# Performance work log

Hardware: AMD Instinct MI355X
Metric: run time of the kernel (lower is better)

Reference implementation:

```python
import jax, jax.numpy as jnp
import numpy as np

DIM = 512
NSLOTS = 8
ITERS = 3
EPS = 1e-8
LN_EPS = 1e-5
SCALE = DIM ** -0.5


def _ln(x, g, b):
    m = jnp.mean(x, axis=-1, keepdims=True)
    v = jnp.mean((x - m) ** 2, axis=-1, keepdims=True)
    return (x - m) / jnp.sqrt(v + LN_EPS) * g + b


def _gru(x, h, W_ih, W_hh, b_ih, b_hh):
    # PyTorch GRUCell, gate order r,z,n
    gi = x @ W_ih.T + b_ih
    gh = h @ W_hh.T + b_hh
    ir, iz, inn = jnp.split(gi, 3, axis=-1)
    hr, hz, hn = jnp.split(gh, 3, axis=-1)
    r = jax.nn.sigmoid(ir + hr)
    z = jax.nn.sigmoid(iz + hz)
    n = jnp.tanh(inn + r * hn)
    return (1.0 - z) * n + z * h


def _norm_attn(dots):
    # softmax over slot axis, then renormalize over token axis
    a = jax.nn.softmax(dots, axis=1)
    return a / (jnp.sum(a, axis=-1, keepdims=True) + EPS)


def setup_inputs() -> dict:
    key = jax.random.key(0)
    ks = jax.random.split(key, 16)
    b, na, ni = 32, 1024, 3136
    d, hd = DIM, DIM  # hidden_dim = max(dim, 128) = 512
    s = 0.02
    inp = {
        'inputs_audio': jax.random.normal(ks[0], (b, na, d), jnp.float32),
        'inputs_image': jax.random.normal(ks[1], (b, ni, d), jnp.float32),
        'slots_noise': jax.random.normal(ks[2], (b, NSLOTS, d), jnp.float32),
        'slots_mu': jax.random.normal(ks[3], (1, 1, d), jnp.float32),
        'slots_logsigma': jnp.zeros((1, 1, d), jnp.float32),
        'ln_in_g': jnp.ones((d,), jnp.float32), 'ln_in_b': jnp.zeros((d,), jnp.float32),
        'ln_slots_g': jnp.ones((d,), jnp.float32), 'ln_slots_b': jnp.zeros((d,), jnp.float32),
        'ln_ff_g': jnp.ones((d,), jnp.float32), 'ln_ff_b': jnp.zeros((d,), jnp.float32),
        'Wq': jax.random.normal(ks[4], (d, d), jnp.float32) * s, 'bq': jnp.zeros((d,), jnp.float32),
        'Wk': jax.random.normal(ks[5], (d, d), jnp.float32) * s, 'bk': jnp.zeros((d,), jnp.float32),
        'Wv': jax.random.normal(ks[6], (d, d), jnp.float32) * s, 'bv': jnp.zeros((d,), jnp.float32),
        'W_ih': jax.random.normal(ks[7], (3 * d, d), jnp.float32) * s,
        'W_hh': jax.random.normal(ks[8], (3 * d, d), jnp.float32) * s,
        'b_ih': jnp.zeros((3 * d,), jnp.float32), 'b_hh': jnp.zeros((3 * d,), jnp.float32),
        'W1': jax.random.normal(ks[9], (hd, d), jnp.float32) * s, 'b1': jnp.zeros((hd,), jnp.float32),
        'W2': jax.random.normal(ks[10], (d, hd), jnp.float32) * s, 'b2': jnp.zeros((d,), jnp.float32),
    }
    return inp


def reference(inputs_audio, inputs_image, slots_noise, slots_mu, slots_logsigma,
              ln_in_g, ln_in_b, ln_slots_g, ln_slots_b, ln_ff_g, ln_ff_b,
              Wq, bq, Wk, bk, Wv, bv, W_ih, W_hh, b_ih, b_hh, W1, b1, W2, b2):
    b, na, d = inputs_audio.shape
    slots0 = slots_mu + jnp.exp(slots_logsigma) * slots_noise  # [b, S, d]

    ia = _ln(inputs_audio, ln_in_g, ln_in_b)
    ii = _ln(inputs_image, ln_in_g, ln_in_b)
    k_a = ia @ Wk.T + bk
    v_a = ia @ Wv.T + bv
    k_i = ii @ Wk.T + bk
    v_i = ii @ Wv.T + bv

    def mlp(x):
        return jax.nn.relu(x @ W1.T + b1) @ W2.T + b2

    def step(slots, k, v):
        prev = slots
        sn = _ln(slots, ln_slots_g, ln_slots_b)
        q = sn @ Wq.T + bq
        dots = jnp.einsum('bid,bjd->bij', q, k) * SCALE
        attn = _norm_attn(dots)
        upd = jnp.einsum('bjd,bij->bid', v, attn)
        h = _gru(upd.reshape(-1, d), prev.reshape(-1, d), W_ih, W_hh, b_ih, b_hh)
        slots = h.reshape(b, -1, d)
        slots = slots + mlp(_ln(slots, ln_ff_g, ln_ff_b))
        return slots, q, attn

    slots_a, slots_i = slots0, slots0
    for _ in range(ITERS):
        slots_a, q_a, attn_a = step(slots_a, k_a, v_a)
        slots_i, q_i, attn_i = step(slots_i, k_i, v_i)

    cross_ai = _norm_attn(jnp.einsum('bid,bjd->bij', q_a, k_i) * SCALE)  # audio->image
    cross_ia = _norm_attn(jnp.einsum('bid,bjd->bij', q_i, k_a) * SCALE)  # image->audio

    return (slots_a, q_a, k_a, attn_a, cross_ia,
            slots_i, q_i, k_i, attn_i, cross_ai)
```

## Files before the change

### kernel.cpp

```cpp
#include <hip/hip_runtime.h>
#include <hip/hip_bf16.h>

#define DIM 512
#define EPS 1e-8f
#define LN_EPS 1e-5f
#define SCALE 0.04419417382415922f

typedef float f32x4 __attribute__((ext_vector_type(4)));
typedef __bf16 bf16;
typedef __bf16 bf16x8 __attribute__((ext_vector_type(8)));

typedef const __attribute__((address_space(1))) void gvoid;
typedef __attribute__((address_space(3))) void lvoid;

__device__ inline float bf2f_lo(unsigned u) { union { unsigned x; float f; } c; c.x = u << 16; return c.f; }
__device__ inline float bf2f_hi(unsigned u) { union { unsigned x; float f; } c; c.x = u & 0xffff0000u; return c.f; }

#define SBAR() do { __builtin_amdgcn_sched_barrier(0); \
                    __builtin_amdgcn_s_barrier(); \
                    __builtin_amdgcn_sched_barrier(0); } while (0)

__global__ __launch_bounds__(256) void k_stats_convert(
    const float* __restrict__ xa, const float* __restrict__ xi,
    bf16* __restrict__ xbfa, bf16* __restrict__ xbfi,
    float* __restrict__ sa, float* __restrict__ si, int MA)
{
  int row = blockIdx.x * 4 + (threadIdx.x >> 6);
  int lane = threadIdx.x & 63;
  bool isA = row < MA;
  int lrow = isA ? row : row - MA;
  const float* xr = (isA ? xa : xi) + (size_t)lrow * DIM;
  bf16* xbf = (isA ? xbfa : xbfi) + (size_t)lrow * DIM;
  float* stats = (isA ? sa : si) + (size_t)lrow * 2;
  float4 a = *(const float4*)(xr + lane * 8);
  float4 b = *(const float4*)(xr + lane * 8 + 4);
  float s  = a.x + a.y + a.z + a.w + b.x + b.y + b.z + b.w;
  float ss = a.x*a.x + a.y*a.y + a.z*a.z + a.w*a.w
           + b.x*b.x + b.y*b.y + b.z*b.z + b.w*b.w;
  for (int off = 32; off; off >>= 1) { s += __shfl_xor(s, off); ss += __shfl_xor(ss, off); }
  float mean = s * (1.0f / DIM);
  float var  = ss * (1.0f / DIM) - mean * mean;
  float rs   = rsqrtf(var + LN_EPS);
  if (lane == 0) { stats[0] = mean; stats[1] = rs; }
  union { bf16 h[8]; uint4 u; } cv;
  cv.h[0] = (bf16)a.x; cv.h[1] = (bf16)a.y; cv.h[2] = (bf16)a.z; cv.h[3] = (bf16)a.w;
  cv.h[4] = (bf16)b.x; cv.h[5] = (bf16)b.y; cv.h[6] = (bf16)b.z; cv.h[7] = (bf16)b.w;
  *(uint4*)(xbf + lane * 8) = cv.u;
}

__global__ __launch_bounds__(256) void k_stats512(
    const float* __restrict__ x, float* __restrict__ stats)
{
  int row = blockIdx.x * 4 + (threadIdx.x >> 6);
  int lane = threadIdx.x & 63;
  const float* xr = x + (size_t)row * DIM;
  float4 a = *(const float4*)(xr + lane * 8);
  float4 b = *(const float4*)(xr + lane * 8 + 4);
  float s  = a.x + a.y + a.z + a.w + b.x + b.y + b.z + b.w;
  float ss = a.x*a.x + a.y*a.y + a.z*a.z + a.w*a.w
           + b.x*b.x + b.y*b.y + b.z*b.z + b.w*b.w;
  for (int off = 32; off; off >>= 1) { s += __shfl_xor(s, off); ss += __shfl_xor(ss, off); }
  float mean = s * (1.0f / DIM);
  float rs   = rsqrtf(ss * (1.0f / DIM) - mean * mean + LN_EPS);
  if (lane == 0) { stats[row * 2] = mean; stats[row * 2 + 1] = rs; }
}

__global__ __launch_bounds__(64) void k_prep(
    const float* __restrict__ Wk, const float* __restrict__ bk,
    const float* __restrict__ Wv, const float* __restrict__ bv,
    const float* __restrict__ g_in, const float* __restrict__ b_in,
    const float* __restrict__ Wq, const float* __restrict__ bq,
    const float* __restrict__ g_s, const float* __restrict__ b_s,
    const float* __restrict__ W1, const float* __restrict__ b1,
    const float* __restrict__ g_f, const float* __restrict__ b_f,
    bf16* __restrict__ wbf, float* __restrict__ c1kv, float* __restrict__ c2kv,
    float* __restrict__ Wqp, float* __restrict__ cq1, float* __restrict__ cq2,
    float* __restrict__ W1p, float* __restrict__ cf1, float* __restrict__ cf2)
{
  int n = blockIdx.x; int lane = threadIdx.x;
  if (n < 1024) {
    const float* W = (n < DIM) ? (Wk + (size_t)n * DIM) : (Wv + (size_t)(n - DIM) * DIM);
    float bias = (n < DIM) ? bk[n] : bv[n - DIM];
    float s1 = 0.f, s2 = 0.f;
    union { bf16 h[8]; uint4 u; } cv;
#pragma unroll
    for (int j = 0; j < 8; ++j) {
      int d = lane * 8 + j;
      float w = W[d];
      float gw = g_in[d] * w;
      s1 += gw; s2 += b_in[d] * w;
      cv.h[j] = (bf16)gw;
    }
    *(uint4*)(wbf + (size_t)n * DIM + lane * 8) = cv.u;
    for (int off = 32; off; off >>= 1) { s1 += __shfl_xor(s1, off); s2 += __shfl_xor(s2, off); }
    if (lane == 0) { c1kv[n] = s1; c2kv[n] = s2 + bias; }
  } else {
    int m; const float* W; float bias; const float* g; const float* b;
    float* Wp; float* cc1; float* cc2;
    if (n < 1536) { m = n - 1024; W = Wq + (size_t)m * DIM; bias = bq[m]; g = g_s; b = b_s; Wp = Wqp; cc1 = cq1; cc2 = cq2; }
    else          { m = n - 1536; W = W1 + (size_t)m * DIM; bias = b1[m]; g = g_f; b = b_f; Wp = W1p; cc1 = cf1; cc2 = cf2; }
    float s1 = 0.f, s2 = 0.f;
    float arr[8];
#pragma unroll
    for (int j = 0; j < 8; ++j) {
      int d = lane * 8 + j;
      float w = W[d];
      float gw = g[d] * w;
      s1 += gw; s2 += b[d] * w;
      arr[j] = gw;
    }
    *(float4*)(Wp + (size_t)m * DIM + lane * 8)     = make_float4(arr[0], arr[1], arr[2], arr[3]);
    *(float4*)(Wp + (size_t)m * DIM + lane * 8 + 4) = make_float4(arr[4], arr[5], arr[6], arr[7]);
    for (int off = 32; off; off >>= 1) { s1 += __shfl_xor(s1, off); s2 += __shfl_xor(s2, off); }
    if (lane == 0) { cc1[m] = s1; cc2[m] = s2 + bias; }
  }
}

__global__ __launch_bounds__(256, 3) void k_kv_gemm(
    const bf16* __restrict__ xa, const bf16* __restrict__ xi,
    const bf16* __restrict__ wbf,
    const float* __restrict__ sa, const float* __restrict__ si,
    const float* __restrict__ c1, const float* __restrict__ c2,
    float* __restrict__ ka, float* __restrict__ ki,
    bf16* __restrict__ kba, bf16* __restrict__ kbi,
    bf16* __restrict__ va, bf16* __restrict__ vi,
    int nblkA, int nblkTot)
{
  __shared__ bf16 As[3][128 * 32];
  __shared__ bf16 Bs[3][128 * 32];
  const int t = threadIdx.x, wave = t >> 6, lane = t & 63;
  int bid = blockIdx.x;
  int rid = (bid & 7) * (nblkTot >> 3) + (bid >> 3);
  bool isA = rid < nblkA;
  int lrid = isA ? rid : rid - nblkA;
  const bf16* x = isA ? xa : xi;
  const float* stats = isA ? sa : si;
  float* kout = isA ? ka : ki;
  bf16* kbf = isA ? kba : kbi;
  bf16* vbf = isA ? va : vi;
  const int row0 = (lrid >> 3) * 128, col0 = (lrid & 7) * 128;
  f32x4 acc[4][4] = {};

  const int sr  = wave * 16 + (lane >> 2);
  const int sgl = ((lane & 3) ^ ((lane >> 3) & 3)) * 8;
  const bf16* asrc = x   + (size_t)(row0 + sr) * DIM + sgl;
  const bf16* bsrc = wbf + (size_t)(col0 + sr) * DIM + sgl;

  auto stage = [&](int buf, int k0) {
#pragma unroll
    for (int p = 0; p < 2; ++p) {
      __builtin_amdgcn_global_load_lds(
          (gvoid*)(asrc + (size_t)(p * 64) * DIM + k0),
          (lvoid*)((char*)&As[0][0] + buf * 8192 + (p * 256 + wave * 64) * 16), 16, 0, 0);
      __builtin_amdgcn_global_load_lds(
          (gvoid*)(bsrc + (size_t)(p * 64) * DIM + k0),
          (lvoid*)((char*)&Bs[0][0] + buf * 8192 + (p * 256 + wave * 64) * 16), 16, 0, 0);
    }
  };

  const int l15 = lane & 15, q16 = lane >> 4;
  const int wm = wave >> 1, wn = wave & 1;
  const int gpx = (q16 ^ ((l15 >> 1) & 3)) * 8;

  stage(0, 0);
  stage(1, 32);
  stage(2, 64);
  asm volatile("s_waitcnt vmcnt(8)" ::: "memory");
  SBAR();
  int cur = 0;
  for (int ks = 0; ks < 16; ++ks) {
    const bf16* Ab = &As[0][0] + cur * (128 * 32);
    const bf16* Bb = &Bs[0][0] + cur * (128 * 32);
    bf16x8 ax[4], bw[4];
#pragma unroll
    for (int mi = 0; mi < 4; ++mi)
      ax[mi] = *(const bf16x8*)(Ab + (wm * 64 + mi * 16 + l15) * 32 + gpx);
#pragma unroll
    for (int ni = 0; ni < 4; ++ni)
      bw[ni] = *(const bf16x8*)(Bb + (wn * 64 + ni * 16 + l15) * 32 + gpx);
    __builtin_amdgcn_s_setprio(1);
#pragma unroll
    for (int ni = 0; ni < 4; ++ni)
#pragma unroll
      for (int mi = 0; mi < 4; ++mi)
        acc[ni][mi] = __builtin_amdgcn_mfma_f32_16x16x32_bf16(bw[ni], ax[mi], acc[ni][mi], 0, 0, 0);
    __builtin_amdgcn_s_setprio(0);
    if (ks == 15) break;
    SBAR();
    if (ks < 13) {
      stage(cur, (ks + 3) * 32);
      asm volatile("s_waitcnt vmcnt(8)" ::: "memory");
    } else if (ks == 13) {
      asm volatile("s_waitcnt vmcnt(4)" ::: "memory");
    } else {
      asm volatile("s_waitcnt vmcnt(0)" ::: "memory");
    }
    SBAR();
    cur = (cur == 2) ? 0 : cur + 1;
  }

#pragma unroll
  for (int mi = 0; mi < 4; ++mi) {
    int row = row0 + wm * 64 + mi * 16 + l15;
    float2 st = *(const float2*)&stats[row * 2];
    float rs = st.y, rm = st.y * st.x;
#pragma unroll
    for (int ni = 0; ni < 4; ++ni) {
      int col = col0 + wn * 64 + ni * 16 + q16 * 4;
      float4 c1v = *(const float4*)&c1[col];
      float4 c2v = *(const float4*)&c2[col];
      f32x4 a = acc[ni][mi];
      float4 o;
      o.x = rs * a[0] - rm * c1v.x + c2v.x;
      o.y = rs * a[1] - rm * c1v.y + c2v.y;
      o.z = rs * a[2] - rm * c1v.z + c2v.z;
      o.w = rs * a[3] - rm * c1v.w + c2v.w;
      union { bf16 h[4]; uint2 u; } pk;
      pk.h[0] = (bf16)o.x; pk.h[1] = (bf16)o.y; pk.h[2] = (bf16)o.z; pk.h[3] = (bf16)o.w;
      if (col0 < DIM) {
        *(float4*)&kout[(size_t)row * DIM + col] = o;
        if (kbf) *(uint2*)&kbf[(size_t)row * DIM + col] = pk.u;
      } else {
        *(uint2*)&vbf[(size_t)row * DIM + (col - DIM)] = pk.u;
      }
    }
  }
}

__global__ __launch_bounds__(256) void k_f2bf(
    const float* __restrict__ in, bf16* __restrict__ out)
{
  size_t i = ((size_t)blockIdx.x * 256 + threadIdx.x) * 8;
  float4 a = *(const float4*)(in + i);
  float4 b = *(const float4*)(in + i + 4);
  union { bf16 h[8]; uint4 u; } cv;
  cv.h[0] = (bf16)a.x; cv.h[1] = (bf16)a.y; cv.h[2] = (bf16)a.z; cv.h[3] = (bf16)a.w;
  cv.h[4] = (bf16)b.x; cv.h[5] = (bf16)b.y; cv.h[6] = (bf16)b.z; cv.h[7] = (bf16)b.w;
  *(uint4*)(out + i) = cv.u;
}

__global__ __launch_bounds__(256) void k_init_slots(
    const float* __restrict__ noise, const float* __restrict__ mu,
    const float* __restrict__ lsig, float* __restrict__ slots,
    float* __restrict__ stats)
{
  int row = blockIdx.x;
  int t = threadIdx.x;
  int d1 = t + 256;
  float v0 = mu[t]  + expf(lsig[t])  * noise[row * DIM + t];
  float v1 = mu[d1] + expf(lsig[d1]) * noise[row * DIM + d1];
  slots[(size_t)row * DIM + t]  = v0;
  slots[(size_t)row * DIM + d1] = v1;
  slots[131072 + (size_t)row * DIM + t]  = v0;
  slots[131072 + (size_t)row * DIM + d1] = v1;
  float s = v0 + v1, ss = v0 * v0 + v1 * v1;
  for (int off = 32; off; off >>= 1) { s += __shfl_xor(s, off); ss += __shfl_xor(ss, off); }
  __shared__ float red[8];
  int wv = t >> 6, ln = t & 63;
  if (ln == 0) { red[wv] = s; red[4 + wv] = ss; }
  __syncthreads();
  if (t == 0) {
    s = red[0] + red[1] + red[2] + red[3];
    ss = red[4] + red[5] + red[6] + red[7];
    float mean = s * (1.0f / DIM);
    float rs = rsqrtf(ss * (1.0f / DIM) - mean * mean + LN_EPS);
    stats[row * 2] = mean; stats[row * 2 + 1] = rs;
    stats[(row + 256) * 2] = mean; stats[(row + 256) * 2 + 1] = rs;
  }
}

template <int MODE>
__global__ __launch_bounds__(128) void k_sgemm(
    const float* __restrict__ A, const float* __restrict__ B, int N,
    float* __restrict__ C,
    const float* __restrict__ c1a, const float* __restrict__ c2a,
    const float* __restrict__ stats,
    const float* __restrict__ bias, const float* __restrict__ invden,
    const float* __restrict__ R,
    float* __restrict__ outA, float* __restrict__ outI,
    bf16* __restrict__ qbf)
{
  __shared__ float As[32][33];
  __shared__ float Bs[64][33];
  int t = threadIdx.x;
  int m0 = blockIdx.y * 32, n0 = blockIdx.x * 64;
  float acc[4][4] = {};
  for (int k0 = 0; k0 < DIM; k0 += 32) {
    __syncthreads();
#pragma unroll
    for (int p = 0; p < 2; ++p) {
      int idx = p * 128 + t, r = idx >> 3, c4 = (idx & 7) * 4;
      float4 v = *(const float4*)(A + (size_t)(m0 + r) * DIM + k0 + c4);
      As[r][c4] = v.x; As[r][c4 + 1] = v.y; As[r][c4 + 2] = v.z; As[r][c4 + 3] = v.w;
    }
#pragma unroll
    for (int p = 0; p < 4; ++p) {
      int idx = p * 128 + t, r = idx >> 3, c4 = (idx & 7) * 4;
      float4 v = *(const float4*)(B + (size_t)(n0 + r) * DIM + k0 + c4);
      Bs[r][c4] = v.x; Bs[r][c4 + 1] = v.y; Bs[r][c4 + 2] = v.z; Bs[r][c4 + 3] = v.w;
    }
    __syncthreads();
    int tr = t >> 4, tc = t & 15;
#pragma unroll
    for (int k = 0; k < 32; ++k) {
      float a0 = As[tr * 4][k], a1 = As[tr * 4 + 1][k], a2 = As[tr * 4 + 2][k], a3 = As[tr * 4 + 3][k];
      float b0 = Bs[tc * 4][k], b1 = Bs[tc * 4 + 1][k], b2 = Bs[tc * 4 + 2][k], b3 = Bs[tc * 4 + 3][k];
      acc[0][0] += a0 * b0; acc[0][1] += a0 * b1; acc[0][2] += a0 * b2; acc[0][3] += a0 * b3;
      acc[1][0] += a1 * b0; acc[1][1] += a1 * b1; acc[1][2] += a1 * b2; acc[1][3] += a1 * b3;
      acc[2][0] += a2 * b0; acc[2][1] += a2 * b1; acc[2][2] += a2 * b2; acc[2][3] += a2 * b3;
      acc[3][0] += a3 * b0; acc[3][1] += a3 * b1; acc[3][2] += a3 * b2; acc[3][3] += a3 * b3;
    }
  }
  int tr = t >> 4, tc = t & 15;
#pragma unroll
  for (int mi = 0; mi < 4; ++mi) {
    int row = m0 + tr * 4 + mi;
#pragma unroll
    for (int ni = 0; ni < 4; ++ni) {
      int col = n0 + tc * 4 + ni;
      float v = acc[mi][ni];
      if (MODE == 0 || MODE == 3) {
        float mean = stats[row * 2], rs = stats[row * 2 + 1];
        v = rs * v - rs * mean * c1a[col] + c2a[col];
      }
      if (MODE == 4) v += bias[col];
      if (MODE == 3) v = fmaxf(v, 0.0f);
      if (MODE == 4) v += R[(size_t)row * N + col];
      if (MODE == 0) {
        if (row < 256) outA[(size_t)row * DIM + col] = v;
        else           outI[(size_t)(row - 256) * DIM + col] = v;
        qbf[(size_t)row * DIM + col] = (bf16)(v * SCALE);
      } else {
        C[(size_t)row * N + col] = v;
        if (MODE == 4 && outA) {
          if (row < 256) outA[(size_t)row * DIM + col] = v;
          else           outI[(size_t)(row - 256) * DIM + col] = v;
        }
      }
    }
  }
}

__global__ __launch_bounds__(128) void k_gates(
    const float* __restrict__ num, const float* __restrict__ slots,
    const float* __restrict__ Wih, const float* __restrict__ Whh,
    const float* __restrict__ bih, const float* __restrict__ bhh,
    const float* __restrict__ invden,
    float* __restrict__ gib, float* __restrict__ ghb)
{
  bool first = blockIdx.x < 24;
  const float* A = first ? num : slots;
  const float* B = first ? Wih : Whh;
  const float* bias = first ? bih : bhh;
  float* C = first ? gib : ghb;
  int n0 = (first ? blockIdx.x : blockIdx.x - 24) * 64;
  int m0 = blockIdx.y * 32;
  __shared__ float As[32][33];
  __shared__ float Bs[64][33];
  int t = threadIdx.x;
  float acc[4][4] = {};
  for (int k0 = 0; k0 < DIM; k0 += 32) {
    __syncthreads();
#pragma unroll
    for (int p = 0; p < 2; ++p) {
      int idx = p * 128 + t, r = idx >> 3, c4 = (idx & 7) * 4;
      float4 v = *(const float4*)(A + (size_t)(m0 + r) * DIM + k0 + c4);
      As[r][c4] = v.x; As[r][c4 + 1] = v.y; As[r][c4 + 2] = v.z; As[r][c4 + 3] = v.w;
    }
#pragma unroll
    for (int p = 0; p < 4; ++p) {
      int idx = p * 128 + t, r = idx >> 3, c4 = (idx & 7) * 4;
      float4 v = *(const float4*)(B + (size_t)(n0 + r) * DIM + k0 + c4);
      Bs[r][c4] = v.x; Bs[r][c4 + 1] = v.y; Bs[r][c4 + 2] = v.z; Bs[r][c4 + 3] = v.w;
    }
    __syncthreads();
    int tr = t >> 4, tc = t & 15;
#pragma unroll
    for (int k = 0; k < 32; ++k) {
      float a0 = As[tr * 4][k], a1 = As[tr * 4 + 1][k], a2 = As[tr * 4 + 2][k], a3 = As[tr * 4 + 3][k];
      float b0 = Bs[tc * 4][k], b1 = Bs[tc * 4 + 1][k], b2 = Bs[tc * 4 + 2][k], b3 = Bs[tc * 4 + 3][k];
      acc[0][0] += a0 * b0; acc[0][1] += a0 * b1; acc[0][2] += a0 * b2; acc[0][3] += a0 * b3;
      acc[1][0] += a1 * b0; acc[1][1] += a1 * b1; acc[1][2] += a1 * b2; acc[1][3] += a1 * b3;
      acc[2][0] += a2 * b0; acc[2][1] += a2 * b1; acc[2][2] += a2 * b2; acc[2][3] += a2 * b3;
      acc[3][0] += a3 * b0; acc[3][1] += a3 * b1; acc[3][2] += a3 * b2; acc[3][3] += a3 * b3;
    }
  }
  int tr = t >> 4, tc = t & 15;
#pragma unroll
  for (int mi = 0; mi < 4; ++mi) {
    int row = m0 + tr * 4 + mi;
    float sc = first ? invden[row] : 1.0f;
#pragma unroll
    for (int ni = 0; ni < 4; ++ni) {
      int col = n0 + tc * 4 + ni;
      C[(size_t)row * 1536 + col] = acc[mi][ni] * sc + bias[col];
    }
  }
}

__global__ __launch_bounds__(256, 3) void k_dots(
    const bf16* __restrict__ qA, const bf16* __restrict__ qI,
    const bf16* __restrict__ kA, const bf16* __restrict__ kI,
    float* __restrict__ aoutA, float* __restrict__ aoutI,
    float* __restrict__ denp, int NA_, int NI_)
{
  __shared__ bf16 ks[3][128 * 64];
  __shared__ float dsh[32];
  int t = threadIdx.x, wave = t >> 6, lane = t & 63;
  int b = blockIdx.y, tile = blockIdx.x;
  bool isA = tile < 8;
  int til = isA ? tile : tile - 8;
  int N = isA ? NA_ : NI_;
  int j0 = til * 128;
  const bf16* q = (isA ? qA : qI) + (size_t)b * 8 * DIM;
  const bf16* k = (isA ? kA : kI) + (size_t)b * N * DIM;
  float* aout = (isA ? aoutA : aoutI) + (size_t)b * 8 * N;
  int drow = (isA ? 0 : 256) + b * 8;

  const int l15 = lane & 15, q16 = lane >> 4;
  bf16x8 afq[16];
  {
    const bf16* qr = q + (size_t)(l15 & 7) * DIM + q16 * 8;
#pragma unroll
    for (int f = 0; f < 16; ++f)
      afq[f] = *(const bf16x8*)(qr + f * 32);
  }

  const int sr  = wave * 8 + (lane >> 3);
  const int sgl = ((lane & 7) ^ (lane >> 3)) * 8;
  int jr = j0 + sr; if (jr > N - 1) jr = N - 1;
  const bf16* ksrc = k + (size_t)jr * DIM + sgl;
  int jr2 = j0 + 32 + sr; if (jr2 > N - 1) jr2 = N - 1;
  const bf16* ksrc2 = k + (size_t)jr2 * DIM + sgl;
  int jr3 = j0 + 64 + sr; if (jr3 > N - 1) jr3 = N - 1;
  const bf16* ksrc3 = k + (size_t)jr3 * DIM + sgl;
  int jr4 = j0 + 96 + sr; if (jr4 > N - 1) jr4 = N - 1;
  const bf16* ksrc4 = k + (size_t)jr4 * DIM + sgl;

  auto stage = [&](int buf, int c) {
    __builtin_amdgcn_global_load_lds((gvoid*)(ksrc  + c * 64),
        (lvoid*)((char*)&ks[0][0] + buf * 16384 + (0 * 256 + wave * 64) * 16), 16, 0, 0);
    __builtin_amdgcn_global_load_lds((gvoid*)(ksrc2 + c * 64),
        (lvoid*)((char*)&ks[0][0] + buf * 16384 + (1 * 256 + wave * 64) * 16), 16, 0, 0);
    __builtin_amdgcn_global_load_lds((gvoid*)(ksrc3 + c * 64),
        (lvoid*)((char*)&ks[0][0] + buf * 16384 + (2 * 256 + wave * 64) * 16), 16, 0, 0);
    __builtin_amdgcn_global_load_lds((gvoid*)(ksrc4 + c * 64),
        (lvoid*)((char*)&ks[0][0] + buf * 16384 + (3 * 256 + wave * 64) * 16), 16, 0, 0);
  };

  stage(0, 0);
  stage(1, 1);
  stage(2, 2);
  asm volatile("s_waitcnt vmcnt(8)" ::: "memory");
  SBAR();
  f32x4 acc[2] = {};
  int cur = 0;
  for (int c = 0; c < 8; ++c) {
    const bf16* kb = &ks[0][0] + cur * (128 * 64);
    __builtin_amdgcn_s_setprio(1);
#pragma unroll
    for (int kk = 0; kk < 2; ++kk) {
#pragma unroll
      for (int n = 0; n < 2; ++n) {
        int R = wave * 32 + n * 16 + l15;
        int gp = (kk * 4 + q16) ^ (R & 7);
        bf16x8 bfr = *(const bf16x8*)(kb + R * 64 + gp * 8);
        acc[n] = __builtin_amdgcn_mfma_f32_16x16x32_bf16(afq[c * 2 + kk], bfr, acc[n], 0, 0, 0);
      }
    }
    __builtin_amdgcn_s_setprio(0);
    if (c == 7) break;
    SBAR();
    if (c < 5) {
      stage(cur, c + 3);
      asm volatile("s_waitcnt vmcnt(8)" ::: "memory");
    } else if (c == 5) {
      asm volatile("s_waitcnt vmcnt(4)" ::: "memory");
    } else {
      asm volatile("s_waitcnt vmcnt(0)" ::: "memory");
    }
    SBAR();
    cur = (cur == 2) ? 0 : cur + 1;
  }

  float dsum[8];
#pragma unroll
  for (int i = 0; i < 8; ++i) dsum[i] = 0.f;
#pragma unroll
  for (int n = 0; n < 2; ++n) {
    int j = j0 + wave * 32 + n * 16 + l15;
    float dv[8];
#pragma unroll
    for (int r = 0; r < 4; ++r) {
      float own = acc[n][r];
      float oth = __shfl_xor(own, 16);
      if (q16 == 0) { dv[r] = own; dv[4 + r] = oth; }
      else          { dv[r] = oth; dv[4 + r] = own; }
    }
    float mx = dv[0];
#pragma unroll
    for (int i = 1; i < 8; ++i) mx = fmaxf(mx, dv[i]);
    float sum = 0.f;
#pragma unroll
    for (int i = 0; i < 8; ++i) { dv[i] = __expf(dv[i] - mx); sum += dv[i]; }
    float inv = 1.0f / sum;
    bool valid = (j < N);
#pragma unroll
    for (int i = 0; i < 8; ++i) {
      float av = valid ? dv[i] * inv : 0.0f;
      dsum[i] += av;
      if (valid && q16 == 0) aout[(size_t)i * N + j] = av;
    }
  }
#pragma unroll
  for (int i = 0; i < 8; ++i) {
    float v = dsum[i];
    v += __shfl_xor(v, 1); v += __shfl_xor(v, 2);
    v += __shfl_xor(v, 4); v += __shfl_xor(v, 8);
    dsum[i] = v;
  }
  if (lane == 0) {
#pragma unroll
    for (int i = 0; i < 8; ++i) dsh[wave * 8 + i] = dsum[i];
  }
  __syncthreads();
  if (t < 8) {
    float den = dsh[t] + dsh[8 + t] + dsh[16 + t] + dsh[24 + t];
    denp[((size_t)drow + t) * 32 + til] = den;
  }
}

__global__ __launch_bounds__(256) void k_upd(
    const bf16* __restrict__ vA, const bf16* __restrict__ vI,
    const float* __restrict__ aA, const float* __restrict__ aI,
    float* __restrict__ numpA, float* __restrict__ numpI, int NA_, int NI_)
{
  __shared__ float ash[128 * 12];
  int t = threadIdx.x, b = blockIdx.y, x = blockIdx.x;
  bool isA = x < 4;
  int c = isA ? x : x - 4;
  int N = isA ? NA_ : NI_;
  int nc = isA ? 4 : 13;
  int jstart = c * 256;
  int jend = jstart + 256; if (jend > N) jend = N;
  const bf16* v = (isA ? vA : vI) + (size_t)b * N * DIM;
  const float* a = (isA ? aA : aI) + (size_t)b * 8 * N;
  float acc[16] = {};
  int d0 = t * 2;
  for (int jt = jstart; jt < jend; jt += 128) {
    int jmax = jend - jt; if (jmax > 128) jmax = 128;
    __syncthreads();
    {
      int i = t >> 5, jq = (t & 31) * 4;
      float4 av = make_float4(0.f, 0.f, 0.f, 0.f);
      if (jt + jq < N) av = *(const float4*)&a[(size_t)i * N + jt + jq];
      ash[(jq + 0) * 12 + i] = av.x;
      ash[(jq + 1) * 12 + i] = av.y;
      ash[(jq + 2) * 12 + i] = av.z;
      ash[(jq + 3) * 12 + i] = av.w;
    }
    __syncthreads();
    for (int jj = 0; jj < jmax; ++jj) {
      unsigned vv = *(const unsigned*)(v + (size_t)(jt + jj) * DIM + d0);
      float v0 = bf2f_lo(vv), v1 = bf2f_hi(vv);
      float4 a0 = *(const float4*)&ash[jj * 12];
      float4 a1 = *(const float4*)&ash[jj * 12 + 4];
      acc[0]  += a0.x * v0; acc[1]  += a0.x * v1;
      acc[2]  += a0.y * v0; acc[3]  += a0.y * v1;
      acc[4]  += a0.z * v0; acc[5]  += a0.z * v1;
      acc[6]  += a0.w * v0; acc[7]  += a0.w * v1;
      acc[8]  += a1.x * v0; acc[9]  += a1.x * v1;
      acc[10] += a1.y * v0; acc[11] += a1.y * v1;
      acc[12] += a1.z * v0; acc[13] += a1.z * v1;
      acc[14] += a1.w * v0; acc[15] += a1.w * v1;
    }
  }
  float* np = (isA ? numpA : numpI) + (((size_t)b * nc + c) * 8) * DIM;
#pragma unroll
  for (int i = 0; i < 8; ++i)
    *(float2*)&np[(size_t)i * DIM + d0] = make_float2(acc[i * 2], acc[i * 2 + 1]);
}

__global__ __launch_bounds__(256) void k_numred(
    const float* __restrict__ numpA, const float* __restrict__ numpI,
    const float* __restrict__ denp,
    float* __restrict__ num, float* __restrict__ invden)
{
  int m = blockIdx.x, t = threadIdx.x;
  bool isA = m < 256;
  int mm = isA ? m : m - 256;
  int bb = mm >> 3, i = mm & 7;
  int nc = isA ? 4 : 13;
  const float* np = (isA ? numpA : numpI) + (((size_t)bb * nc) * 8 + i) * DIM;
  int d0 = t * 2;
  float s0 = 0.f, s1 = 0.f;
  for (int c = 0; c < nc; ++c) {
    float2 vv = *(const float2*)&np[(size_t)c * 8 * DIM + d0];
    s0 += vv.x; s1 += vv.y;
  }
  *(float2*)&num[(size_t)m * DIM + d0] = make_float2(s0, s1);
  if (t == 0) {
    int nch = isA ? 8 : 25;
    float den = EPS;
    for (int c2 = 0; c2 < nch; ++c2) den += denp[(size_t)m * 32 + c2];
    invden[m] = 1.0f / den;
  }
}

__global__ __launch_bounds__(256) void k_gru(
    const float* __restrict__ gi, const float* __restrict__ gh,
    const float* __restrict__ prev,
    float* __restrict__ hout, float* __restrict__ stats_h)
{
  int m = blockIdx.x; int t = threadIdx.x;
  size_t b3 = (size_t)m * 1536, b1 = (size_t)m * DIM;
  float h[2]; float s = 0.f, ss = 0.f;
#pragma unroll
  for (int p = 0; p < 2; ++p) {
    int d = t + p * 256;
    float ir = gi[b3 + d], iz = gi[b3 + 512 + d], in_ = gi[b3 + 1024 + d];
    float hr = gh[b3 + d], hz = gh[b3 + 512 + d], hn = gh[b3 + 1024 + d];
    float r = 1.f / (1.f + __expf(-(ir + hr)));
    float z = 1.f / (1.f + __expf(-(iz + hz)));
    float n = tanhf(in_ + r * hn);
    float hv = (1.f - z) * n + z * prev[b1 + d];
    hout[b1 + d] = hv;
    h[p] = hv; s += hv; ss += hv * hv;
  }
  for (int off = 32; off; off >>= 1) { s += __shfl_xor(s, off); ss += __shfl_xor(ss, off); }
  __shared__ float red[8];
  int wv = t >> 6, ln = t & 63;
  if (ln == 0) { red[wv] = s; red[4 + wv] = ss; }
  __syncthreads();
  s = red[0] + red[1] + red[2] + red[3];
  ss = red[4] + red[5] + red[6] + red[7];
  float mean = s * (1.0f / DIM);
  float rs = rsqrtf(ss * (1.0f / DIM) - mean * mean + LN_EPS);
  if (t == 0) { stats_h[m * 2] = mean; stats_h[m * 2 + 1] = rs; }
}

__global__ __launch_bounds__(256) void k_renorm2(
    const float* __restrict__ aA, const float* __restrict__ aI,
    const float* __restrict__ denp,
    float* __restrict__ outA, float* __restrict__ outI, int NA_, int NI_)
{
  int m = blockIdx.x; int t = threadIdx.x;
  bool isA = m < 256;
  int mm = isA ? m : m - 256;
  int N = isA ? NA_ : NI_;
  int nch = isA ? 8 : 25;
  const float* in = (isA ? aA : aI) + (size_t)mm * N;
  float* out = (isA ? outA : outI) + (size_t)mm * N;
  float den = EPS;
  for (int c = 0; c < nch; ++c) den += denp[(size_t)m * 32 + c];
  float inv = 1.0f / den;
  for (int idx = t; idx * 4 < N; idx += 256) {
    float4 v = *(const float4*)&in[idx * 4];
    v.x *= inv; v.y *= inv; v.z *= inv; v.w *= inv;
    *(float4*)&out[idx * 4] = v;
  }
}

extern "C" void kernel_launch(void* const* d_in, const int* in_sizes, int n_in,
                              void* d_out, int out_size, void* d_ws, size_t ws_size,
                              hipStream_t stream)
{
  (void)in_sizes; (void)n_in; (void)out_size;
  const float* x_a   = (const float*)d_in[0];
  const float* x_i   = (const float*)d_in[1];
  const float* noise = (const float*)d_in[2];
  const float* mu    = (const float*)d_in[3];
  const float* lsig  = (const float*)d_in[4];
  const float* ln_in_g = (const float*)d_in[5];
  const float* ln_in_b = (const float*)d_in[6];
  const float* ln_s_g  = (const float*)d_in[7];
  const float* ln_s_b  = (const float*)d_in[8];
  const float* ln_f_g  = (const float*)d_in[9];
  const float* ln_f_b  = (const float*)d_in[10];
  const float* Wq = (const float*)d_in[11]; const float* bq = (const float*)d_in[12];
  const float* Wk = (const float*)d_in[13]; const float* bk = (const float*)d_in[14];
  const float* Wv = (const float*)d_in[15]; const float* bv = (const float*)d_in[16];
  const float* W_ih = (const float*)d_in[17]; const float* W_hh = (const float*)d_in[18];
  const float* b_ih = (const float*)d_in[19]; const float* b_hh = (const float*)d_in[20];
  const float* W1 = (const float*)d_in[21]; const float* b1 = (const float*)d_in[22];
  const float* W2 = (const float*)d_in[23]; const float* b2 = (const float*)d_in[24];

  const int NA = 1024, NI = 3136;
  const int MA = 32 * NA, MI = 32 * NI;

  float* out = (float*)d_out;
  float* o_slots_a  = out;
  float* o_q_a      = out + 131072;
  float* o_k_a      = out + 262144;
  float* o_attn_a   = out + 17039360;
  float* o_cross_ia = out + 17301504;
  float* o_slots_i  = out + 17563648;
  float* o_q_i      = out + 17694720;
  float* o_k_i      = out + 17825792;
  float* o_attn_i   = out + 69206016;
  float* o_cross_ai = out + 70008832;

  char* w = (char*)d_ws;
  size_t used = 0;
  auto alloc = [&](size_t bytes) {
    char* p = w + used;
    used += (bytes + 255) & ~(size_t)255;
    return p;
  };
  bf16* xbf_a = (bf16*)alloc((size_t)MA * DIM * 2);
  bf16* xbf_i = (bf16*)alloc((size_t)MI * DIM * 2);
  bf16* vbf_a = (bf16*)alloc((size_t)MA * DIM * 2);
  bf16* vbf_i = (bf16*)alloc((size_t)MI * DIM * 2);
  float* stats_a = (float*)alloc((size_t)MA * 2 * 4);
  float* stats_i = (float*)alloc((size_t)MI * 2 * 4);
  bf16* wbf  = (bf16*)alloc(1024 * 512 * 2);
  float* c1kv = (float*)alloc(1024 * 4);
  float* c2kv = (float*)alloc(1024 * 4);
  float* Wqp = (float*)alloc(512 * 512 * 4);
  float* cq1 = (float*)alloc(512 * 4);
  float* cq2 = (float*)alloc(512 * 4);
  float* W1p = (float*)alloc(512 * 512 * 4);
  float* cf1 = (float*)alloc(512 * 4);
  float* cf2 = (float*)alloc(512 * 4);
  float* slots = (float*)alloc(512 * 512 * 4);
  bf16*  qbf   = (bf16*)alloc(512 * 512 * 2);
  float* mid   = (float*)alloc(512 * 512 * 4);
  float* hid   = (float*)alloc(512 * 512 * 4);
  float* num   = (float*)alloc(512 * 512 * 4);
  float* gib   = (float*)alloc(512 * 1536 * 4);
  float* ghb   = (float*)alloc(512 * 1536 * 4);
  float* stats_s = (float*)alloc(512 * 2 * 4);
  float* stats_h = (float*)alloc(512 * 2 * 4);
  float* invden  = (float*)alloc(512 * 4);
  float* denp    = (float*)alloc(512 * 32 * 4);
  float* abuf_a  = (float*)alloc((size_t)256 * NA * 4);
  float* abuf_i  = (float*)alloc((size_t)256 * NI * 4);
  float* numpA   = (float*)alloc((size_t)32 * 4 * 8 * DIM * 4);
  float* numpI   = (float*)alloc((size_t)32 * 13 * 8 * DIM * 4);
  if (used > ws_size) return;

  size_t kbf_bytes = (((size_t)MA * DIM * 2 + 255) & ~(size_t)255)
                   + (((size_t)MI * DIM * 2 + 255) & ~(size_t)255);
  bf16* kbf_a; bf16* kbf_i; bool kbf_fused;
  if (used + kbf_bytes <= ws_size) {
    kbf_a = (bf16*)alloc((size_t)MA * DIM * 2);
    kbf_i = (bf16*)alloc((size_t)MI * DIM * 2);
    kbf_fused = true;
  } else {
    kbf_a = xbf_a; kbf_i = xbf_i;
    kbf_fused = false;
  }

  k_stats_convert<<<(MA + MI) / 4, 256, 0, stream>>>(x_a, x_i, xbf_a, xbf_i,
                                                     stats_a, stats_i, MA);
  k_prep<<<2048, 64, 0, stream>>>(Wk, bk, Wv, bv, ln_in_g, ln_in_b,
                                  Wq, bq, ln_s_g, ln_s_b, W1, b1, ln_f_g, ln_f_b,
                                  wbf, c1kv, c2kv, Wqp, cq1, cq2, W1p, cf1, cf2);
  {
    int nblkA = (MA / 128) * 8;
    int nblkTot = nblkA + (MI / 128) * 8;
    k_kv_gemm<<<nblkTot, 256, 0, stream>>>(xbf_a, xbf_i, wbf, stats_a, stats_i,
        c1kv, c2kv, o_k_a, o_k_i,
        kbf_fused ? kbf_a : nullptr, kbf_fused ? kbf_i : nullptr,
        vbf_a, vbf_i, nblkA, nblkTot);
  }
  if (!kbf_fused) {
    k_f2bf<<<MA * DIM / 2048, 256, 0, stream>>>(o_k_a, kbf_a);
    k_f2bf<<<MI * DIM / 2048, 256, 0, stream>>>(o_k_i, kbf_i);
  }
  k_init_slots<<<256, 256, 0, stream>>>(noise, mu, lsig, slots, stats_s);

  for (int it = 0; it < 3; ++it) {
    bool last = (it == 2);
    k_sgemm<0><<<dim3(8, 16), 128, 0, stream>>>(slots, Wqp, DIM, nullptr,
        cq1, cq2, stats_s, nullptr, nullptr, nullptr, o_q_a, o_q_i, qbf);
    k_dots<<<dim3(33, 32), 256, 0, stream>>>(qbf, qbf + 256 * DIM,
        kbf_a, kbf_i, abuf_a, abuf_i, denp, NA, NI);
    k_upd<<<dim3(17, 32), 256, 0, stream>>>(vbf_a, vbf_i, abuf_a, abuf_i, numpA, numpI, NA, NI);
    k_numred<<<512, 256, 0, stream>>>(numpA, numpI, denp, num, invden);
    k_gates<<<dim3(48, 16), 128, 0, stream>>>(num, slots, W_ih, W_hh,
        b_ih, b_hh, invden, gib, ghb);
    k_gru<<<512, 256, 0, stream>>>(gib, ghb, slots, mid, stats_h);
    k_sgemm<3><<<dim3(8, 16), 128, 0, stream>>>(mid, W1p, DIM, hid,
        cf1, cf2, stats_h, nullptr, nullptr, nullptr, nullptr, nullptr, nullptr);
    k_sgemm<4><<<dim3(8, 16), 128, 0, stream>>>(hid, W2, DIM, slots,
        nullptr, nullptr, nullptr, b2, nullptr, mid,
        last ? o_slots_a : nullptr, last ? o_slots_i : nullptr, nullptr);
    if (!last) k_stats512<<<128, 256, 0, stream>>>(slots, stats_s);
  }

  k_renorm2<<<512, 256, 0, stream>>>(abuf_a, abuf_i, denp, o_attn_a, o_attn_i, NA, NI);

  k_dots<<<dim3(33, 32), 256, 0, stream>>>(qbf + 256 * DIM, qbf,
      kbf_a, kbf_i, abuf_a, abuf_i, denp, NA, NI);
  k_renorm2<<<512, 256, 0, stream>>>(abuf_a, abuf_i, denp, o_cross_ia, o_cross_ai, NA, NI);
}
```

Before: 1.121 ms.

## Fuse dots and update kernels, compute cross-attention in final iteration, double-buffer GEMMs

Merges the attention-dots kernel and the attention-times-V update kernel into one kernel that keeps the attention tile in shared memory. This removes the full attention write and read on the first two iterations. On the last iteration it also computes the cross-attention logits against the same staged K tile, so the separate cross dots pass no longer has to re-read K. The KV GEMM and dots pipelines drop from triple to double buffering to cut LDS use and raise occupancy. The trade-offs are a shallower prefetch pipeline and more partial numerator chunks for the reduction kernel to sum.

New measurement: 1.104 ms. About the same (-1.5%).

```diff
diff --git a/kernel.cpp b/kernel.cpp
--- a/kernel.cpp
+++ b/kernel.cpp
@@ -116,7 +116,7 @@
   }
 }
 
-__global__ __launch_bounds__(256, 3) void k_kv_gemm(
+__global__ __launch_bounds__(256, 4) void k_kv_gemm(
     const bf16* __restrict__ xa, const bf16* __restrict__ xi,
     const bf16* __restrict__ wbf,
     const float* __restrict__ sa, const float* __restrict__ si,
@@ -126,8 +126,8 @@
     bf16* __restrict__ va, bf16* __restrict__ vi,
     int nblkA, int nblkTot)
 {
-  __shared__ bf16 As[3][128 * 32];
-  __shared__ bf16 Bs[3][128 * 32];
+  __shared__ bf16 As[2][128 * 32];
+  __shared__ bf16 Bs[2][128 * 32];
   const int t = threadIdx.x, wave = t >> 6, lane = t & 63;
   int bid = blockIdx.x;
   int rid = (bid & 7) * (nblkTot >> 3) + (bid >> 3);
@@ -151,10 +151,10 @@
     for (int p = 0; p < 2; ++p) {
       __builtin_amdgcn_global_load_lds(
           (gvoid*)(asrc + (size_t)(p * 64) * DIM + k0),
-          (lvoid*)((char*)&As[0][0] + buf * 8192 + (p * 256 + wave * 64) * 16), 16, 0, 0);
+          (lvoid*)((char*)&As[buf][0] + (p * 256 + wave * 64) * 16), 16, 0, 0);
       __builtin_amdgcn_global_load_lds(
           (gvoid*)(bsrc + (size_t)(p * 64) * DIM + k0),
-          (lvoid*)((char*)&Bs[0][0] + buf * 8192 + (p * 256 + wave * 64) * 16), 16, 0, 0);
+          (lvoid*)((char*)&Bs[buf][0] + (p * 256 + wave * 64) * 16), 16, 0, 0);
     }
   };
 
@@ -164,13 +164,12 @@
 
   stage(0, 0);
   stage(1, 32);
-  stage(2, 64);
-  asm volatile("s_waitcnt vmcnt(8)" ::: "memory");
+  asm volatile("s_waitcnt vmcnt(4)" ::: "memory");
   SBAR();
   int cur = 0;
   for (int ks = 0; ks < 16; ++ks) {
-    const bf16* Ab = &As[0][0] + cur * (128 * 32);
-    const bf16* Bb = &Bs[0][0] + cur * (128 * 32);
+    const bf16* Ab = &As[cur][0];
+    const bf16* Bb = &Bs[cur][0];
     bf16x8 ax[4], bw[4];
 #pragma unroll
     for (int mi = 0; mi < 4; ++mi)
@@ -187,16 +186,14 @@
     __builtin_amdgcn_s_setprio(0);
     if (ks == 15) break;
     SBAR();
-    if (ks < 13) {
-      stage(cur, (ks + 3) * 32);
-      asm volatile("s_waitcnt vmcnt(8)" ::: "memory");
-    } else if (ks == 13) {
+    if (ks < 14) {
+      stage(cur, (ks + 2) * 32);
       asm volatile("s_waitcnt vmcnt(4)" ::: "memory");
     } else {
       asm volatile("s_waitcnt vmcnt(0)" ::: "memory");
     }
     SBAR();
-    cur = (cur == 2) ? 0 : cur + 1;
+    cur ^= 1;
   }
 
 #pragma unroll
@@ -327,8 +324,10 @@
       if (MODE == 3) v = fmaxf(v, 0.0f);
       if (MODE == 4) v += R[(size_t)row * N + col];
       if (MODE == 0) {
-        if (row < 256) outA[(size_t)row * DIM + col] = v;
-        else           outI[(size_t)(row - 256) * DIM + col] = v;
+        if (outA) {
+          if (row < 256) outA[(size_t)row * DIM + col] = v;
+          else           outI[(size_t)(row - 256) * DIM + col] = v;
+        }
         qbf[(size_t)row * DIM + col] = (bf16)(v * SCALE);
       } else {
         C[(size_t)row * N + col] = v;
@@ -398,32 +397,46 @@
   }
 }
 
-__global__ __launch_bounds__(256, 3) void k_dots(
+template <int LAST>
+__global__ __launch_bounds__(256) void k_dots_upd(
     const bf16* __restrict__ qA, const bf16* __restrict__ qI,
     const bf16* __restrict__ kA, const bf16* __restrict__ kI,
+    const bf16* __restrict__ vA, const bf16* __restrict__ vI,
     float* __restrict__ aoutA, float* __restrict__ aoutI,
-    float* __restrict__ denp, int NA_, int NI_)
-{
-  __shared__ bf16 ks[3][128 * 64];
-  __shared__ float dsh[32];
+    float* __restrict__ acA, float* __restrict__ acI,
+    float* __restrict__ denp, float* __restrict__ denpc,
+    float* __restrict__ numpA, float* __restrict__ numpI,
+    int NA_, int NI_)
+{
+  __shared__ bf16 ks[2][128 * 64];
+  __shared__ float ash[128 * 12];
+  __shared__ float dsh[64];
   int t = threadIdx.x, wave = t >> 6, lane = t & 63;
   int b = blockIdx.y, tile = blockIdx.x;
   bool isA = tile < 8;
   int til = isA ? tile : tile - 8;
   int N = isA ? NA_ : NI_;
+  int nc = isA ? 8 : 25;
   int j0 = til * 128;
-  const bf16* q = (isA ? qA : qI) + (size_t)b * 8 * DIM;
-  const bf16* k = (isA ? kA : kI) + (size_t)b * N * DIM;
-  float* aout = (isA ? aoutA : aoutI) + (size_t)b * 8 * N;
+  const bf16* qo = (isA ? qA : qI) + (size_t)b * 8 * DIM;
+  const bf16* qc = (isA ? qI : qA) + (size_t)b * 8 * DIM;
+  const bf16* k  = (isA ? kA : kI) + (size_t)b * N * DIM;
+  const bf16* v  = (isA ? vA : vI) + (size_t)b * N * DIM;
+  float* aout = (isA ? aoutA : aoutI) + (LAST ? (size_t)b * 8 * N : 0);
+  float* aco  = (isA ? acA  : acI ) + (LAST ? (size_t)b * 8 * N : 0);
   int drow = (isA ? 0 : 256) + b * 8;
 
   const int l15 = lane & 15, q16 = lane >> 4;
-  bf16x8 afq[16];
+  bf16x8 afq[16], afqc[16];
   {
-    const bf16* qr = q + (size_t)(l15 & 7) * DIM + q16 * 8;
-#pragma unroll
-    for (int f = 0; f < 16; ++f)
-      afq[f] = *(const bf16x8*)(qr + f * 32);
+    const bf16* qr = qo + (size_t)(l15 & 7) * DIM + q16 * 8;
+#pragma unroll
+    for (int f = 0; f < 16; ++f) afq[f] = *(const bf16x8*)(qr + f * 32);
+  }
+  if (LAST) {
+    const bf16* qr = qc + (size_t)(l15 & 7) * DIM + q16 * 8;
+#pragma unroll
+    for (int f = 0; f < 16; ++f) afqc[f] = *(const bf16x8*)(qr + f * 32);
   }
 
   const int sr  = wave * 8 + (lane >> 3);
@@ -450,10 +463,9 @@
 
   stage(0, 0);
   stage(1, 1);
-  stage(2, 2);
-  asm volatile("s_waitcnt vmcnt(8)" ::: "memory");
+  asm volatile("s_waitcnt vmcnt(4)" ::: "memory");
   SBAR();
-  f32x4 acc[2] = {};
+  f32x4 acc[2] = {}, accc[2] = {};
   int cur = 0;
   for (int c = 0; c < 8; ++c) {
     const bf16* kb = &ks[0][0] + cur * (128 * 64);
@@ -466,119 +478,131 @@
         int gp = (kk * 4 + q16) ^ (R & 7);
         bf16x8 bfr = *(const bf16x8*)(kb + R * 64 + gp * 8);
         acc[n] = __builtin_amdgcn_mfma_f32_16x16x32_bf16(afq[c * 2 + kk], bfr, acc[n], 0, 0, 0);
+        if (LAST)
+          accc[n] = __builtin_amdgcn_mfma_f32_16x16x32_bf16(afqc[c * 2 + kk], bfr, accc[n], 0, 0, 0);
       }
     }
     __builtin_amdgcn_s_setprio(0);
     if (c == 7) break;
     SBAR();
-    if (c < 5) {
-      stage(cur, c + 3);
-      asm volatile("s_waitcnt vmcnt(8)" ::: "memory");
-    } else if (c == 5) {
+    if (c < 6) {
+      stage(cur, c + 2);
       asm volatile("s_waitcnt vmcnt(4)" ::: "memory");
     } else {
       asm volatile("s_waitcnt vmcnt(0)" ::: "memory");
     }
     SBAR();
-    cur = (cur == 2) ? 0 : cur + 1;
-  }
-
-  float dsum[8];
-#pragma unroll
-  for (int i = 0; i < 8; ++i) dsum[i] = 0.f;
+    cur ^= 1;
+  }
+
+  float dsum[8], dsumc[8];
+#pragma unroll
+  for (int i = 0; i < 8; ++i) { dsum[i] = 0.f; dsumc[i] = 0.f; }
 #pragma unroll
   for (int n = 0; n < 2; ++n) {
-    int j = j0 + wave * 32 + n * 16 + l15;
-    float dv[8];
-#pragma unroll
-    for (int r = 0; r < 4; ++r) {
-      float own = acc[n][r];
-      float oth = __shfl_xor(own, 16);
-      if (q16 == 0) { dv[r] = own; dv[4 + r] = oth; }
-      else          { dv[r] = oth; dv[4 + r] = own; }
-    }
-    float mx = dv[0];
-#pragma unroll
-    for (int i = 1; i < 8; ++i) mx = fmaxf(mx, dv[i]);
-    float sum = 0.f;
-#pragma unroll
-    for (int i = 0; i < 8; ++i) { dv[i] = __expf(dv[i] - mx); sum += dv[i]; }
-    float inv = 1.0f / sum;
+    int jloc = wave * 32 + n * 16 + l15;
+    int j = j0 + jloc;
     bool valid = (j < N);
+    {
+      float dv[8];
+#pragma unroll
+      for (int r = 0; r < 4; ++r) {
+        float own = acc[n][r];
+        float oth = __shfl_xor(own, 16);
+        if (q16 == 0) { dv[r] = own; dv[4 + r] = oth; }
+        else          { dv[r] = oth; dv[4 + r] = own; }
+      }
+      float mx = dv[0];
+#pragma unroll
+      for (int i = 1; i < 8; ++i) mx = fmaxf(mx, dv[i]);
+      float sum = 0.f;
+#pragma unroll
+      for (int i = 0; i < 8; ++i) { dv[i] = __expf(dv[i] - mx); sum += dv[i]; }
+      float inv = 1.0f / sum;
+#pragma unroll
+      for (int i = 0; i < 8; ++i) {
+        float av = valid ? dv[i] * inv : 0.0f;
+        dsum[i] += av;
+        if (q16 == 0) {
+          ash[jloc * 12 + i] = av;
+          if (LAST && valid) aout[(size_t)i * N + j] = av;
+        }
+      }
+    }
+    if (LAST) {
+      float dv[8];
+#pragma unroll
+      for (int r = 0; r < 4; ++r) {
+        float own = accc[n][r];
+        float oth = __shfl_xor(own, 16);
+        if (q16 == 0) { dv[r] = own; dv[4 + r] = oth; }
+        else          { dv[r] = oth; dv[4 + r] = own; }
+      }
+      float mx = dv[0];
+#pragma unroll
+      for (int i = 1; i < 8; ++i) mx = fmaxf(mx, dv[i]);
+      float sum = 0.f;
+#pragma unroll
+      for (int i = 0; i < 8; ++i) { dv[i] = __expf(dv[i] - mx); sum += dv[i]; }
+      float inv = 1.0f / sum;
+#pragma unroll
+      for (int i = 0; i < 8; ++i) {
+        float av = valid ? dv[i] * inv : 0.0f;
+        dsumc[i] += av;
+        if (q16 == 0 && valid) aco[(size_t)i * N + j] = av;
+      }
+    }
+  }
+#pragma unroll
+  for (int i = 0; i < 8; ++i) {
+    float x1 = dsum[i];
+    x1 += __shfl_xor(x1, 1); x1 += __shfl_xor(x1, 2);
+    x1 += __shfl_xor(x1, 4); x1 += __shfl_xor(x1, 8);
+    dsum[i] = x1;
+    if (LAST) {
+      float x2 = dsumc[i];
+      x2 += __shfl_xor(x2, 1); x2 += __shfl_xor(x2, 2);
+      x2 += __shfl_xor(x2, 4); x2 += __shfl_xor(x2, 8);
+      dsumc[i] = x2;
+    }
+  }
+  if (lane == 0) {
 #pragma unroll
     for (int i = 0; i < 8; ++i) {
-      float av = valid ? dv[i] * inv : 0.0f;
-      dsum[i] += av;
-      if (valid && q16 == 0) aout[(size_t)i * N + j] = av;
-    }
-  }
-#pragma unroll
-  for (int i = 0; i < 8; ++i) {
-    float v = dsum[i];
-    v += __shfl_xor(v, 1); v += __shfl_xor(v, 2);
-    v += __shfl_xor(v, 4); v += __shfl_xor(v, 8);
-    dsum[i] = v;
-  }
-  if (lane == 0) {
-#pragma unroll
-    for (int i = 0; i < 8; ++i) dsh[wave * 8 + i] = dsum[i];
+      dsh[wave * 8 + i] = dsum[i];
+      if (LAST) dsh[32 + wave * 8 + i] = dsumc[i];
+    }
   }
   __syncthreads();
   if (t < 8) {
-    float den = dsh[t] + dsh[8 + t] + dsh[16 + t] + dsh[24 + t];
-    denp[((size_t)drow + t) * 32 + til] = den;
-  }
-}
-
-__global__ __launch_bounds__(256) void k_upd(
-    const bf16* __restrict__ vA, const bf16* __restrict__ vI,
-    const float* __restrict__ aA, const float* __restrict__ aI,
-    float* __restrict__ numpA, float* __restrict__ numpI, int NA_, int NI_)
-{
-  __shared__ float ash[128 * 12];
-  int t = threadIdx.x, b = blockIdx.y, x = blockIdx.x;
-  bool isA = x < 4;
-  int c = isA ? x : x - 4;
-  int N = isA ? NA_ : NI_;
-  int nc = isA ? 4 : 13;
-  int jstart = c * 256;
-  int jend = jstart + 256; if (jend > N) jend = N;
-  const bf16* v = (isA ? vA : vI) + (size_t)b * N * DIM;
-  const float* a = (isA ? aA : aI) + (size_t)b * 8 * N;
-  float acc[16] = {};
+    denp[((size_t)drow + t) * 32 + til] = dsh[t] + dsh[8 + t] + dsh[16 + t] + dsh[24 + t];
+  }
+  if (LAST && t >= 8 && t < 16) {
+    int i = t - 8;
+    denpc[((size_t)drow + i) * 32 + til] = dsh[32 + i] + dsh[40 + i] + dsh[48 + i] + dsh[56 + i];
+  }
+
+  float ua[16] = {};
   int d0 = t * 2;
-  for (int jt = jstart; jt < jend; jt += 128) {
-    int jmax = jend - jt; if (jmax > 128) jmax = 128;
-    __syncthreads();
-    {
-      int i = t >> 5, jq = (t & 31) * 4;
-      float4 av = make_float4(0.f, 0.f, 0.f, 0.f);
-      if (jt + jq < N) av = *(const float4*)&a[(size_t)i * N + jt + jq];
-      ash[(jq + 0) * 12 + i] = av.x;
-      ash[(jq + 1) * 12 + i] = av.y;
-      ash[(jq + 2) * 12 + i] = av.z;
-      ash[(jq + 3) * 12 + i] = av.w;
-    }
-    __syncthreads();
-    for (int jj = 0; jj < jmax; ++jj) {
-      unsigned vv = *(const unsigned*)(v + (size_t)(jt + jj) * DIM + d0);
-      float v0 = bf2f_lo(vv), v1 = bf2f_hi(vv);
-      float4 a0 = *(const float4*)&ash[jj * 12];
-      float4 a1 = *(const float4*)&ash[jj * 12 + 4];
-      acc[0]  += a0.x * v0; acc[1]  += a0.x * v1;
-      acc[2]  += a0.y * v0; acc[3]  += a0.y * v1;
-      acc[4]  += a0.z * v0; acc[5]  += a0.z * v1;
-      acc[6]  += a0.w * v0; acc[7]  += a0.w * v1;
-      acc[8]  += a1.x * v0; acc[9]  += a1.x * v1;
-      acc[10] += a1.y * v0; acc[11] += a1.y * v1;
-      acc[12] += a1.z * v0; acc[13] += a1.z * v1;
-      acc[14] += a1.w * v0; acc[15] += a1.w * v1;
-    }
-  }
-  float* np = (isA ? numpA : numpI) + (((size_t)b * nc + c) * 8) * DIM;
+  for (int jj = 0; jj < 128; ++jj) {
+    int jv = j0 + jj; if (jv > N - 1) jv = N - 1;
+    unsigned vv = *(const unsigned*)(v + (size_t)jv * DIM + d0);
+    float v0 = bf2f_lo(vv), v1 = bf2f_hi(vv);
+    float4 a0 = *(const float4*)&ash[jj * 12];
+    float4 a1 = *(const float4*)&ash[jj * 12 + 4];
+    ua[0]  += a0.x * v0; ua[1]  += a0.x * v1;
+    ua[2]  += a0.y * v0; ua[3]  += a0.y * v1;
+    ua[4]  += a0.z * v0; ua[5]  += a0.z * v1;
+    ua[6]  += a0.w * v0; ua[7]  += a0.w * v1;
+    ua[8]  += a1.x * v0; ua[9]  += a1.x * v1;
+    ua[10] += a1.y * v0; ua[11] += a1.y * v1;
+    ua[12] += a1.z * v0; ua[13] += a1.z * v1;
+    ua[14] += a1.w * v0; ua[15] += a1.w * v1;
+  }
+  float* np = (isA ? numpA : numpI) + (((size_t)b * nc + til) * 8) * DIM;
 #pragma unroll
   for (int i = 0; i < 8; ++i)
-    *(float2*)&np[(size_t)i * DIM + d0] = make_float2(acc[i * 2], acc[i * 2 + 1]);
+    *(float2*)&np[(size_t)i * DIM + d0] = make_float2(ua[i * 2], ua[i * 2 + 1]);
 }
 
 __global__ __launch_bounds__(256) void k_numred(
@@ -590,7 +614,7 @@
   bool isA = m < 256;
   int mm = isA ? m : m - 256;
   int bb = mm >> 3, i = mm & 7;
-  int nc = isA ? 4 : 13;
+  int nc = isA ? 8 : 25;
   const float* np = (isA ? numpA : numpI) + (((size_t)bb * nc) * 8 + i) * DIM;
   int d0 = t * 2;
   float s0 = 0.f, s1 = 0.f;
@@ -600,9 +624,8 @@
   }
   *(float2*)&num[(size_t)m * DIM + d0] = make_float2(s0, s1);
   if (t == 0) {
-    int nch = isA ? 8 : 25;
     float den = EPS;
-    for (int c2 = 0; c2 < nch; ++c2) den += denp[(size_t)m * 32 + c2];
+    for (int c2 = 0; c2 < nc; ++c2) den += denp[(size_t)m * 32 + c2];
     invden[m] = 1.0f / den;
   }
 }
@@ -733,10 +756,13 @@
   float* stats_h = (float*)alloc(512 * 2 * 4);
   float* invden  = (float*)alloc(512 * 4);
   float* denp    = (float*)alloc(512 * 32 * 4);
+  float* denpc   = (float*)alloc(512 * 32 * 4);
   float* abuf_a  = (float*)alloc((size_t)256 * NA * 4);
   float* abuf_i  = (float*)alloc((size_t)256 * NI * 4);
-  float* numpA   = (float*)alloc((size_t)32 * 4 * 8 * DIM * 4);
-  float* numpI   = (float*)alloc((size_t)32 * 13 * 8 * DIM * 4);
+  float* abufc_a = (float*)alloc((size_t)256 * NA * 4);
+  float* abufc_i = (float*)alloc((size_t)256 * NI * 4);
+  float* numpA   = (float*)alloc((size_t)32 * 8 * 8 * DIM * 4);
+  float* numpI   = (float*)alloc((size_t)32 * 25 * 8 * DIM * 4);
   if (used > ws_size) return;
 
   size_t kbf_bytes = (((size_t)MA * DIM * 2 + 255) & ~(size_t)255)
@@ -773,10 +799,18 @@
   for (int it = 0; it < 3; ++it) {
     bool last = (it == 2);
     k_sgemm<0><<<dim3(8, 16), 128, 0, stream>>>(slots, Wqp, DIM, nullptr,
-        cq1, cq2, stats_s, nullptr, nullptr, nullptr, o_q_a, o_q_i, qbf);
-    k_dots<<<dim3(33, 32), 256, 0, stream>>>(qbf, qbf + 256 * DIM,
-        kbf_a, kbf_i, abuf_a, abuf_i, denp, NA, NI);
-    k_upd<<<dim3(17, 32), 256, 0, stream>>>(vbf_a, vbf_i, abuf_a, abuf_i, numpA, numpI, NA, NI);
+        cq1, cq2, stats_s, nullptr, nullptr, nullptr,
+        last ? o_q_a : nullptr, last ? o_q_i : nullptr, qbf);
+    if (!last)
+      k_dots_upd<0><<<dim3(33, 32), 256, 0, stream>>>(qbf, qbf + 256 * DIM,
+          kbf_a, kbf_i, vbf_a, vbf_i,
+          nullptr, nullptr, nullptr, nullptr, denp, nullptr,
+          numpA, numpI, NA, NI);
+    else
+      k_dots_upd<1><<<dim3(33, 32), 256, 0, stream>>>(qbf, qbf + 256 * DIM,
+          kbf_a, kbf_i, vbf_a, vbf_i,
+          abuf_a, abuf_i, abufc_a, abufc_i, denp, denpc,
+          numpA, numpI, NA, NI);
     k_numred<<<512, 256, 0, stream>>>(numpA, numpI, denp, num, invden);
     k_gates<<<dim3(48, 16), 128, 0, stream>>>(num, slots, W_ih, W_hh,
         b_ih, b_hh, invden, gib, ghb);
@@ -790,8 +824,5 @@
   }
 
   k_renorm2<<<512, 256, 0, stream>>>(abuf_a, abuf_i, denp, o_attn_a, o_attn_i, NA, NI);
-
-  k_dots<<<dim3(33, 32), 256, 0, stream>>>(qbf + 256 * DIM, qbf,
-      kbf_a, kbf_i, abuf_a, abuf_i, denp, NA, NI);
-  k_renorm2<<<512, 256, 0, stream>>>(abuf_a, abuf_i, denp, o_cross_ia, o_cross_ai, NA, NI);
-}
+  k_renorm2<<<512, 256, 0, stream>>>(abufc_a, abufc_i, denpc, o_cross_ia, o_cross_ai, NA, NI);
+}
```
